# Optimization experiments

Hardware: AMD Instinct MI355X
Metric: run time of the kernel (lower is better)

The kernel has to match this reference:

```python
import jax, jax.numpy as jnp
import numpy as np

B = 4096
IN_DIMS = (3, 32, 32)      # in_numel = 3072
OUT_DIMS = (64, 16, 16)    # out_numel = 16384
IN_NUMEL = int(np.prod(IN_DIMS))
OUT_NUMEL = int(np.prod(OUT_DIMS))


def setup_inputs() -> dict:
    key = jax.random.key(0)
    k1, k2, k3, k4 = jax.random.split(key, 4)
    x = jax.random.normal(k1, (B,) + IN_DIMS, dtype=jnp.float32)
    # Cached composed linear operator (out_numel x in_numel); scale ~1/sqrt(fan_in)
    cached_matrix = jax.random.normal(k2, (OUT_NUMEL, IN_NUMEL), dtype=jnp.float32) / np.sqrt(IN_NUMEL)
    cached_matrix_extra = jax.random.uniform(k3, (1,), dtype=jnp.float32) + 0.5
    cached_tensor_extra = jax.random.normal(k4, (IN_NUMEL, IN_NUMEL), dtype=jnp.float32) / IN_NUMEL
    return {
        "x": x,
        "cached_matrix": cached_matrix,
        "cached_matrix_extra": cached_matrix_extra,
        "cached_tensor_extra": cached_tensor_extra,
    }


def reference(x, cached_matrix, cached_matrix_extra, cached_tensor_extra):
    batches = x.shape[0]
    # input_as_matrix: [in_numel, B]
    X = x.reshape(batches, -1).T
    # input_as_matrix_extra: L2 norm per column -> [1, B]
    X_extra = jnp.linalg.norm(X, ord=2, axis=0, keepdims=True)
    # output_as_matrix = M @ X : [out_numel, B]
    Y = jnp.matmul(cached_matrix, X)
    # output_as_matrix_extra = s * ||x|| + sum((T @ X) * X, axis=0)
    Y_extra = cached_matrix_extra * X_extra + jnp.sum(jnp.matmul(cached_tensor_extra, X) * X, axis=0, keepdims=True)
    Y = Y / Y_extra
    return Y.T.reshape(batches, *OUT_DIMS)
```

## Files before the change

kernel.cpp:

```cpp
#include <hip/hip_runtime.h>
#include <hip/hip_bf16.h>

typedef __attribute__((ext_vector_type(8))) short bf16x8;
typedef __attribute__((ext_vector_type(4))) short bf16x4;
typedef __attribute__((ext_vector_type(4))) float f32x4;

#define DEV __device__ __forceinline__

static constexpr int BATCH = 4096;
static constexpr int KDIM  = 3072;
static constexpr int NOUT  = 16384;

DEV unsigned short f2bf(float f) {
  union { float f; unsigned int u; } v; v.f = f;
  unsigned int u = v.u;
  u += 0x7fffu + ((u >> 16) & 1u);
  return (unsigned short)(u >> 16);
}

DEV float bf2f(unsigned short h) {
  union { unsigned int u; float f; } v;
  v.u = ((unsigned int)h) << 16;
  return v.f;
}

DEV bf16x4 pk4(float4 v) {
  bf16x4 o;
  o[0] = (short)f2bf(v.x); o[1] = (short)f2bf(v.y);
  o[2] = (short)f2bf(v.z); o[3] = (short)f2bf(v.w);
  return o;
}

__global__ __launch_bounds__(256) void prep_cvtT_kernel(
    const float* __restrict__ x, unsigned short* __restrict__ xbf,
    float* __restrict__ nrm,
    const float* __restrict__ T, unsigned short* __restrict__ tbf) {
  __shared__ float red[4];
  const int bid = blockIdx.x;
  const int t = threadIdx.x;
  if (bid < BATCH) {
    const float* row = x + (size_t)bid * KDIM;
    unsigned short* orow = xbf + (size_t)bid * KDIM;
    float ss = 0.f;
#pragma unroll
    for (int i = 0; i < 3; ++i) {
      const int c = i * 256 + t;
      float4 v = reinterpret_cast<const float4*>(row)[c];
      ss += v.x * v.x + v.y * v.y + v.z * v.z + v.w * v.w;
      reinterpret_cast<bf16x4*>(orow)[c] = pk4(v);
    }
#pragma unroll
    for (int off = 32; off > 0; off >>= 1) ss += __shfl_down(ss, off, 64);
    if ((t & 63) == 0) red[t >> 6] = ss;
    __syncthreads();
    if (t == 0) nrm[bid] = sqrtf(red[0] + red[1] + red[2] + red[3]);
  } else {
    const int cb = bid - BATCH;
    const size_t n4 = (size_t)KDIM * KDIM / 4;
    const size_t stride = 1024 * 256;
    for (size_t i = (size_t)cb * 256 + t; i < n4; i += stride) {
      float4 v = reinterpret_cast<const float4*>(T)[i];
      reinterpret_cast<bf16x4*>(tbf)[i] = pk4(v);
    }
  }
}

__global__ __launch_bounds__(256) void finalize_ye_kernel(
    const float* __restrict__ nrm, const float* __restrict__ partial,
    const float* __restrict__ sp, float* __restrict__ ye) {
  const int b = blockIdx.x * blockDim.x + threadIdx.x;
  if (b >= BATCH) return;
  float qv = 0.f;
#pragma unroll
  for (int i = 0; i < 48; ++i) qv += partial[(size_t)b * 48 + i];
  ye[b] = sp[0] * nrm[b] + qv;
}

static constexpr int BK8 = 64;

#define LDSE(BUF, OP, HALF) ((BUF)*32768 + (OP)*16384 + (HALF)*8192)

#define STAGE8(OP, HALF, S, BUF)                                             \
  {                                                                          \
    const unsigned short* gb_ = (OP) ? Bm : A;                               \
    const int gr0_ = ((OP) ? col0 : row0) + (HALF)*128;                      \
    _Pragma("unroll")                                                        \
    for (int j_ = 0; j_ < 2; ++j_) {                                         \
      const int row_ = j_*64 + wid*8 + (lane >> 3);                          \
      const int le_  = ((lane & 7)*8) ^ ((row_ & 7) << 3);                   \
      __builtin_amdgcn_global_load_lds(                                      \
        (const __attribute__((address_space(1))) unsigned int*)(const void*) \
          (gb_ + (size_t)(gr0_ + row_)*KDIM + (S)*BK8 + le_),                \
        (__attribute__((address_space(3))) unsigned int*)(void*)             \
          (lds + LDSE(BUF, OP, HALF) + j_*4096 + wid*512),                   \
        16, 0, 0);                                                           \
    }                                                                        \
  }

#define LOADA8(P, QM, DST)                                                   \
  _Pragma("unroll")                                                          \
  for (int mi = 0; mi < 4; ++mi) {                                           \
    const int r_ = wm*64 + mi*16 + (lane & 15);                              \
    const int xv_ = (r_ & 7) << 3;                                           \
    _Pragma("unroll")                                                        \
    for (int ks = 0; ks < 2; ++ks)                                           \
      DST[mi][ks] = *reinterpret_cast<const bf16x8*>(                        \
          lds + LDSE(P, 0, QM) + ((r_*64 + ks*32 + (lane >> 4)*8) ^ xv_));   \
  }

#define LOADB8(P, QN, DST)                                                   \
  _Pragma("unroll")                                                          \
  for (int ni = 0; ni < 2; ++ni) {                                           \
    const int r_ = wn*32 + ni*16 + (lane & 15);                              \
    const int xv_ = (r_ & 7) << 3;                                           \
    _Pragma("unroll")                                                        \
    for (int ks = 0; ks < 2; ++ks)                                           \
      DST[ni][ks] = *reinterpret_cast<const bf16x8*>(                        \
          lds + LDSE(P, 1, QN) + ((r_*64 + ks*32 + (lane >> 4)*8) ^ xv_));   \
  }

#define MMA8(QM, QN, ASRC, BSRC)                                             \
  __builtin_amdgcn_s_setprio(1);                                             \
  _Pragma("unroll")                                                          \
  for (int mi = 0; mi < 4; ++mi)                                             \
    _Pragma("unroll")                                                        \
    for (int ni = 0; ni < 2; ++ni)                                           \
      _Pragma("unroll")                                                      \
      for (int ks = 0; ks < 2; ++ks)                                         \
        acc[(QM)*4 + mi][(QN)*2 + ni] =                                      \
            __builtin_amdgcn_mfma_f32_16x16x32_bf16(                         \
                ASRC[mi][ks], BSRC[ni][ks], acc[(QM)*4 + mi][(QN)*2 + ni],   \
                0, 0, 0);                                                    \
  __builtin_amdgcn_s_setprio(0);

#define VMW(N)                                                               \
  asm volatile("s_waitcnt vmcnt(" #N ")" ::: "memory");                      \
  __builtin_amdgcn_sched_barrier(0)

#define BARR __builtin_amdgcn_s_barrier()

#define TILE9(P, T)                                                          \
  LOADA8(P, 0, aft); LOADB8(P, 0, bft0);                                     \
  STAGE8(1, 1, (T)+1, (P)^1);                                                \
  BARR;                                                                      \
  STAGE8(1, 0, (T)+1, (P)^1);                                                \
  MMA8(0, 0, aft, bft0);                                                     \
  LOADB8(P, 1, bft1);                                                        \
  BARR;                                                                      \
  STAGE8(0, 0, (T)+2, P);                                                    \
  MMA8(0, 1, aft, bft1);                                                     \
  LOADA8(P, 1, aft);                                                         \
  BARR;                                                                      \
  MMA8(1, 1, aft, bft1);                                                     \
  BARR;                                                                      \
  STAGE8(0, 1, (T)+2, P);                                                    \
  MMA8(1, 0, aft, bft0);                                                     \
  VMW(4);                                                                    \
  BARR;

#define LGKMW8 asm volatile("s_waitcnt lgkmcnt(8)" ::: "memory")

#define TILE8Q(P, T)                                                         \
  LOADA8(P, 0, aft); LOADB8(P, 0, bft0);                                     \
  STAGE8(1, 1, (T)+1, (P)^1);                                                \
  LGKMW8;                                                                    \
  BARR; MMA8(0, 0, aft, bft0); BARR;                                         \
  LOADB8(P, 1, bft1);                                                        \
  STAGE8(1, 0, (T)+1, (P)^1);                                                \
  BARR; MMA8(0, 1, aft, bft1); BARR;                                         \
  LOADA8(P, 1, aft);                                                         \
  STAGE8(0, 0, (T)+2, P);                                                    \
  BARR; MMA8(1, 1, aft, bft1); BARR;                                         \
  STAGE8(0, 1, (T)+2, P);                                                    \
  BARR; MMA8(1, 0, aft, bft0); VMW(4); BARR;

#define PROLOG8Q(T0)                                                         \
  STAGE8(0, 0, (T0), 0); STAGE8(1, 0, (T0), 0);                              \
  STAGE8(0, 1, (T0), 0); STAGE8(1, 1, (T0), 0);                              \
  STAGE8(0, 0, (T0)+1, 1); STAGE8(0, 1, (T0)+1, 1);                          \
  VMW(4);                                                                    \
  BARR;

#define TAIL8Q(TE)                                                           \
  LOADA8(0, 0, aft); LOADB8(0, 0, bft0);                                     \
  STAGE8(1, 1, (TE)+1, 1);                                                   \
  BARR; MMA8(0, 0, aft, bft0); BARR;                                         \
  LOADB8(0, 1, bft1);                                                        \
  STAGE8(1, 0, (TE)+1, 1);                                                   \
  BARR; MMA8(0, 1, aft, bft1); BARR;                                         \
  LOADA8(0, 1, aft);                                                         \
  BARR; MMA8(1, 1, aft, bft1); BARR;                                         \
  MMA8(1, 0, aft, bft0); VMW(0); BARR;                                       \
  LOADA8(1, 0, aft); LOADB8(1, 0, bft0);                                     \
  BARR; MMA8(0, 0, aft, bft0); BARR;                                         \
  LOADB8(1, 1, bft1);                                                        \
  BARR; MMA8(0, 1, aft, bft1); BARR;                                         \
  LOADA8(1, 1, aft);                                                         \
  BARR; MMA8(1, 1, aft, bft1); BARR;                                         \
  MMA8(1, 0, aft, bft0);

__global__ __launch_bounds__(512) void gemm8_kernel(
    const unsigned short* __restrict__ A,
    const unsigned short* __restrict__ Bm,
    const float* __restrict__ ye,
    float* __restrict__ out) {
  __shared__ unsigned short lds[65536];
  const int t = threadIdx.x;
  const int lane = t & 63, wid = t >> 6;
  const int wm = wid >> 2, wn = wid & 3;

  const int bid = blockIdx.x;
  const int xcd = bid & 7, r = bid >> 3;
  const int by = r >> 3;
  const int bx = xcd * 8 + (r & 7);
  const int row0 = by * 256, col0 = bx * 256;

  f32x4 acc[8][4];
#pragma unroll
  for (int i = 0; i < 8; ++i)
#pragma unroll
    for (int j = 0; j < 4; ++j) acc[i][j] = (f32x4){0.f, 0.f, 0.f, 0.f};

  bf16x8 aft[4][2], bft0[2][2], bft1[2][2];

  STAGE8(1, 1, 0, 0); STAGE8(1, 0, 0, 0);
  STAGE8(0, 0, 0, 0); STAGE8(0, 1, 0, 0);
  STAGE8(0, 0, 1, 1); STAGE8(0, 1, 1, 1);
  VMW(4);
  BARR;

#pragma unroll 1
  for (int i = 0; i < 23; ++i) {
    const int t0 = 2 * i;
    TILE9(0, t0);
    TILE9(1, t0 + 1);
  }

  LOADA8(0, 0, aft); LOADB8(0, 0, bft0);
  STAGE8(1, 1, 47, 1);
  BARR;
  STAGE8(1, 0, 47, 1);
  MMA8(0, 0, aft, bft0);
  LOADB8(0, 1, bft1);
  BARR;
  MMA8(0, 1, aft, bft1);
  LOADA8(0, 1, aft);
  BARR;
  MMA8(1, 1, aft, bft1);
  BARR;
  MMA8(1, 0, aft, bft0);
  VMW(0);
  BARR;
  LOADA8(1, 0, aft); LOADB8(1, 0, bft0);
  BARR;
  MMA8(0, 0, aft, bft0);
  LOADB8(1, 1, bft1);
  BARR;
  MMA8(0, 1, aft, bft1);
  LOADA8(1, 1, aft);
  BARR;
  MMA8(1, 1, aft, bft1);
  BARR;
  MMA8(1, 0, aft, bft0);

#pragma unroll
  for (int am = 0; am < 8; ++am) {
#pragma unroll
    for (int j = 0; j < 4; ++j) {
      const int b = row0 + (am >> 2) * 128 + wm * 64 + (am & 3) * 16 +
                    (lane >> 4) * 4 + j;
      const float rr = 1.0f / ye[b];
      float* orow = out + (size_t)b * NOUT + col0;
#pragma unroll
      for (int an = 0; an < 4; ++an)
        orow[(an >> 1) * 128 + wn * 32 + (an & 1) * 16 + (lane & 15)] =
            acc[am][an][j] * rr;
    }
  }
}

#define CVT_EVEN(PT)                                                         \
  if (DOCVT) {                                                               \
    cb0 = Mf4[cvb + (size_t)(((PT)+1)*3    )*512];                           \
    cb1 = Mf4[cvb + (size_t)(((PT)+1)*3 + 1)*512];                           \
    cb2 = Mf4[cvb + (size_t)(((PT)+1)*3 + 2)*512];                           \
    Mb4[cvb + (size_t)((PT)*3    )*512] = pk4(ca0);                          \
    Mb4[cvb + (size_t)((PT)*3 + 1)*512] = pk4(ca1);                          \
    Mb4[cvb + (size_t)((PT)*3 + 2)*512] = pk4(ca2);                          \
  }
#define CVT_ODD(PT)                                                          \
  if (DOCVT) {                                                               \
    ca0 = Mf4[cvb + (size_t)(((PT)+1)*3    )*512];                           \
    ca1 = Mf4[cvb + (size_t)(((PT)+1)*3 + 1)*512];                           \
    if ((PT) != 9) ca2 = Mf4[cvb + (size_t)(((PT)+1)*3 + 2)*512];            \
    Mb4[cvb + (size_t)((PT)*3    )*512] = pk4(cb0);                          \
    Mb4[cvb + (size_t)((PT)*3 + 1)*512] = pk4(cb1);                          \
    Mb4[cvb + (size_t)((PT)*3 + 2)*512] = pk4(cb2);                          \
  }

template <int DOCVT>
__global__ __launch_bounds__(512) void qform8_kernel(
    const unsigned short* __restrict__ A,
    const unsigned short* __restrict__ Bm,
    float* __restrict__ partial,
    const float* __restrict__ Mf,
    unsigned short* __restrict__ Mbf) {
  __shared__ unsigned short lds[65536];
  const int t = threadIdx.x;
  const int lane = t & 63, wid = t >> 6;
  const int wm = wid >> 2, wn = wid & 3;

  const int bid = blockIdx.x;
  const int wgid = (bid & 7) * 96 + (bid >> 3);
  const int jt = wgid / 64;
  const int rem = wgid % 64;
  const int bt = rem >> 2;
  const int ks4 = rem & 3;
  const int row0 = bt * 256, col0 = jt * 256;
  const int k0t = ks4 * 12;

  f32x4 acc[8][4];
#pragma unroll
  for (int i = 0; i < 8; ++i)
#pragma unroll
    for (int j = 0; j < 4; ++j) acc[i][j] = (f32x4){0.f, 0.f, 0.f, 0.f};

  bf16x8 aft[4][2], bft0[2][2], bft1[2][2];

  const float4* Mf4 = reinterpret_cast<const float4*>(Mf);
  bf16x4* Mb4 = reinterpret_cast<bf16x4*>(Mbf);
  const size_t cvb = (size_t)bid * 16384 + t;
  float4 ca0, ca1, ca2, cb0, cb1, cb2;
  if (DOCVT) {
    ca0 = Mf4[cvb];
    ca1 = Mf4[cvb + 512];
    ca2 = Mf4[cvb + 1024];
  }

  PROLOG8Q(k0t);
#pragma unroll 1
  for (int i = 0; i < 5; ++i) {
    const int t0 = k0t + 2 * i;
    CVT_EVEN(2 * i);
    TILE8Q(0, t0);
    CVT_ODD(2 * i + 1);
    TILE8Q(1, t0 + 1);
  }
  if (DOCVT) {
    Mb4[cvb + (size_t)(30) * 512] = pk4(ca0);
    Mb4[cvb + (size_t)(31) * 512] = pk4(ca1);
  }
  TAIL8Q(k0t + 10);

  float* sred = reinterpret_cast<float*>(lds);
#pragma unroll
  for (int am = 0; am < 8; ++am) {
#pragma unroll
    for (int j = 0; j < 4; ++j) {
      const int b = row0 + (am >> 2) * 128 + wm * 64 + (am & 3) * 16 +
                    (lane >> 4) * 4 + j;
      float s = 0.f;
#pragma unroll
      for (int an = 0; an < 4; ++an) {
        const int col = col0 + (an >> 1) * 128 + wn * 32 + (an & 1) * 16 +
                        (lane & 15);
        s += acc[am][an][j] * bf2f(A[(size_t)b * KDIM + col]);
      }
      s += __shfl_xor(s, 1, 64);
      s += __shfl_xor(s, 2, 64);
      s += __shfl_xor(s, 4, 64);
      s += __shfl_xor(s, 8, 64);
      if ((lane & 15) == 0)
        sred[wid * 128 + am * 16 + j * 4 + (lane >> 4)] = s;
    }
  }
  __syncthreads();
  if (t < 256) {
    const int wmI = t >> 7, idx = t & 127;
    const int am = idx >> 4, j = (idx >> 2) & 3, lp = idx & 3;
    const int b = row0 + (am >> 2) * 128 + wmI * 64 + (am & 3) * 16 + lp * 4 + j;
    float s = 0.f;
#pragma unroll
    for (int w2 = 0; w2 < 4; ++w2) s += sred[(wmI * 4 + w2) * 128 + idx];
    partial[(size_t)b * 48 + jt * 4 + ks4] = s;
  }
}

__global__ __launch_bounds__(256) void main_gemm_kernel(
    const unsigned short* __restrict__ A,
    const float* __restrict__ Bf,
    const float* __restrict__ ye,
    float* __restrict__ out) {
  __shared__ unsigned short ldsA[128 * 32];
  __shared__ unsigned short ldsB[128 * 32];
  const int t = threadIdx.x;
  const int lane = t & 63;
  const int wv = t >> 6;
  const int wr = wv >> 1, wc = wv & 1;
  const int col0 = blockIdx.x * 128;
  const int row0 = blockIdx.y * 128;

  f32x4 acc[4][4];
#pragma unroll
  for (int i = 0; i < 4; ++i)
#pragma unroll
    for (int j = 0; j < 4; ++j) acc[i][j] = (f32x4){0.f, 0.f, 0.f, 0.f};

  const unsigned short* aBase = A + (size_t)row0 * KDIM;
  const float* bfBase = Bf + (size_t)col0 * KDIM;
  const int ldsoff0 = (t & ~63) * 8;

  for (int k0 = 0; k0 < KDIM; k0 += 32) {
    __syncthreads();
#pragma unroll
    for (int i = 0; i < 2; ++i) {
      const int c = i * 256 + t;
      const unsigned short* ga = aBase + (size_t)(c >> 2) * KDIM + (k0 + (c & 3) * 8);
      __builtin_amdgcn_global_load_lds(
          (const __attribute__((address_space(1))) unsigned int*)(const void*)ga,
          (__attribute__((address_space(3))) unsigned int*)(void*)(ldsA + i * 2048 + ldsoff0),
          16, 0, 0);
    }
#pragma unroll
    for (int i = 0; i < 2; ++i) {
      const int c = i * 256 + t;
      const int r = c >> 1, ko = (c & 1) * 16;
      const float* gp = bfBase + (size_t)r * KDIM + k0 + ko;
      unsigned short tmp[16];
#pragma unroll
      for (int q = 0; q < 4; ++q) {
        float4 v = reinterpret_cast<const float4*>(gp)[q];
        tmp[q * 4 + 0] = f2bf(v.x); tmp[q * 4 + 1] = f2bf(v.y);
        tmp[q * 4 + 2] = f2bf(v.z); tmp[q * 4 + 3] = f2bf(v.w);
      }
#pragma unroll
      for (int q = 0; q < 2; ++q)
        *reinterpret_cast<bf16x8*>(&ldsB[r * 32 + ko + q * 8]) =
            *reinterpret_cast<const bf16x8*>(&tmp[q * 8]);
    }
    __syncthreads();
    bf16x8 af[4], bfr[4];
#pragma unroll
    for (int mi = 0; mi < 4; ++mi)
      af[mi] = *reinterpret_cast<const bf16x8*>(
          &ldsA[(wr * 64 + mi * 16 + (lane & 15)) * 32 + (lane >> 4) * 8]);
#pragma unroll
    for (int ni = 0; ni < 4; ++ni)
      bfr[ni] = *reinterpret_cast<const bf16x8*>(
          &ldsB[(wc * 64 + ni * 16 + (lane & 15)) * 32 + (lane >> 4) * 8]);
#pragma unroll
    for (int mi = 0; mi < 4; ++mi)
#pragma unroll
      for (int ni = 0; ni < 4; ++ni)
        acc[mi][ni] = __builtin_amdgcn_mfma_f32_16x16x32_bf16(af[mi], bfr[ni], acc[mi][ni], 0, 0, 0);
  }

#pragma unroll
  for (int mi = 0; mi < 4; ++mi) {
#pragma unroll
    for (int j = 0; j < 4; ++j) {
      const int b = row0 + wr * 64 + mi * 16 + (lane >> 4) * 4 + j;
      const float rr = 1.0f / ye[b];
      float* orow = out + (size_t)b * NOUT + col0 + wc * 64 + (lane & 15);
#pragma unroll
      for (int ni = 0; ni < 4; ++ni) orow[ni * 16] = acc[mi][ni][j] * rr;
    }
  }
}

extern "C" void kernel_launch(void* const* d_in, const int* in_sizes, int n_in,
                              void* d_out, int out_size, void* d_ws, size_t ws_size,
                              hipStream_t stream) {
  (void)in_sizes; (void)n_in; (void)out_size;
  const float* x  = (const float*)d_in[0];
  const float* M  = (const float*)d_in[1];
  const float* sc = (const float*)d_in[2];
  const float* T  = (const float*)d_in[3];
  float* out = (float*)d_out;
  char* ws = (char*)d_ws;

  size_t off = 0;
  auto wsalloc = [&](size_t bytes) -> void* {
    void* p = ws + off;
    off += (bytes + 255) & ~(size_t)255;
    return p;
  };
  unsigned short* Xbf = (unsigned short*)wsalloc((size_t)BATCH * KDIM * 2);
  unsigned short* Tbf = (unsigned short*)wsalloc((size_t)KDIM * KDIM * 2);
  float* nrm = (float*)wsalloc((size_t)BATCH * 4);
  float* ye  = (float*)wsalloc((size_t)BATCH * 4);
  float* partial = (float*)wsalloc((size_t)BATCH * 48 * 4);
  unsigned short* Mbf = (unsigned short*)wsalloc((size_t)NOUT * KDIM * 2);
  const bool useMbf = (off <= ws_size);

  prep_cvtT_kernel<<<BATCH + 1024, 256, 0, stream>>>(x, Xbf, nrm, T, Tbf);
  if (useMbf)
    qform8_kernel<1><<<768, 512, 0, stream>>>(Xbf, Tbf, partial, M, Mbf);
  else
    qform8_kernel<0><<<768, 512, 0, stream>>>(Xbf, Tbf, partial, M, Mbf);
  finalize_ye_kernel<<<BATCH / 256, 256, 0, stream>>>(nrm, partial, sc, ye);
  if (useMbf)
    gemm8_kernel<<<1024, 512, 0, stream>>>(Xbf, Mbf, ye, out);
  else
    main_gemm_kernel<<<dim3(NOUT / 128, BATCH / 128), 256, 0, stream>>>(
        Xbf, M, ye, out);
}
```

Before: 558.2 us.

## Replace 8-wave quadrant-pipelined GEMM with simple double-buffered full-tile loop

Replaces the main bf16 GEMM's intricate quadrant-interleaved schedule, which staged and computed tile halves with many barriers, with a plain double-buffered loop. Each iteration prefetches the next K tile into the other LDS buffer via global_load_lds, waits, then runs the full 8x4 MFMA block per wave in two k-steps. The wave-to-tile mapping changes so each wave owns a contiguous 128x64 output region. The goal is to cut barrier count and scheduling complexity, at the cost of less fine-grained overlap between LDS loads and MFMAs and a full barrier each iteration.

```diff
diff --git a/kernel.cpp b/kernel.cpp
--- a/kernel.cpp
+++ b/kernel.cpp
@@ -139,24 +139,7 @@
 
 #define BARR __builtin_amdgcn_s_barrier()
 
-#define TILE9(P, T)                                                          \
-  LOADA8(P, 0, aft); LOADB8(P, 0, bft0);                                     \
-  STAGE8(1, 1, (T)+1, (P)^1);                                                \
-  BARR;                                                                      \
-  STAGE8(1, 0, (T)+1, (P)^1);                                                \
-  MMA8(0, 0, aft, bft0);                                                     \
-  LOADB8(P, 1, bft1);                                                        \
-  BARR;                                                                      \
-  STAGE8(0, 0, (T)+2, P);                                                    \
-  MMA8(0, 1, aft, bft1);                                                     \
-  LOADA8(P, 1, aft);                                                         \
-  BARR;                                                                      \
-  MMA8(1, 1, aft, bft1);                                                     \
-  BARR;                                                                      \
-  STAGE8(0, 1, (T)+2, P);                                                    \
-  MMA8(1, 0, aft, bft0);                                                     \
-  VMW(4);                                                                    \
-  BARR;
+#define SBAR0 __builtin_amdgcn_sched_barrier(0)
 
 #define LGKMW8 asm volatile("s_waitcnt lgkmcnt(8)" ::: "memory")
 
@@ -199,7 +182,54 @@
   BARR; MMA8(1, 1, aft, bft1); BARR;                                         \
   MMA8(1, 0, aft, bft0);
 
-__global__ __launch_bounds__(512) void gemm8_kernel(
+#define LDS2(BUF, OP) ((BUF)*32768 + (OP)*16384)
+
+#define STAGE2(OP, S, BUF)                                                   \
+  {                                                                          \
+    const unsigned short* gb_ = (OP) ? Bm : A;                               \
+    const int gr0_ = (OP) ? col0 : row0;                                     \
+    _Pragma("unroll")                                                        \
+    for (int j_ = 0; j_ < 4; ++j_) {                                         \
+      const int row_ = j_*64 + wid*8 + (lane >> 3);                          \
+      const int le_  = ((lane & 7)*8) ^ ((row_ & 7) << 3);                   \
+      __builtin_amdgcn_global_load_lds(                                      \
+        (const __attribute__((address_space(1))) unsigned int*)(const void*) \
+          (gb_ + (size_t)(gr0_ + row_)*KDIM + (S)*BK8 + le_),                \
+        (__attribute__((address_space(3))) unsigned int*)(void*)             \
+          (lds + LDS2(BUF, OP) + j_*4096 + wid*512),                         \
+        16, 0, 0);                                                           \
+    }                                                                        \
+  }
+
+#define LOADA2(P, KS)                                                        \
+  _Pragma("unroll")                                                          \
+  for (int mi = 0; mi < 8; ++mi) {                                           \
+    const int r_ = wm*128 + mi*16 + (lane & 15);                             \
+    aft[mi] = *reinterpret_cast<const bf16x8*>(                              \
+        lds + LDS2(P, 0) +                                                   \
+        ((r_*64 + (KS)*32 + (lane >> 4)*8) ^ ((r_ & 7) << 3)));              \
+  }
+
+#define LOADB2(P, KS)                                                        \
+  _Pragma("unroll")                                                          \
+  for (int ni = 0; ni < 4; ++ni) {                                           \
+    const int r_ = wn*64 + ni*16 + (lane & 15);                              \
+    bft[ni] = *reinterpret_cast<const bf16x8*>(                              \
+        lds + LDS2(P, 1) +                                                   \
+        ((r_*64 + (KS)*32 + (lane >> 4)*8) ^ ((r_ & 7) << 3)));              \
+  }
+
+#define MMA2                                                                 \
+  __builtin_amdgcn_s_setprio(1);                                             \
+  _Pragma("unroll")                                                          \
+  for (int mi = 0; mi < 8; ++mi)                                             \
+    _Pragma("unroll")                                                        \
+    for (int ni = 0; ni < 4; ++ni)                                           \
+      acc[mi][ni] = __builtin_amdgcn_mfma_f32_16x16x32_bf16(                 \
+          aft[mi], bft[ni], acc[mi][ni], 0, 0, 0);                           \
+  __builtin_amdgcn_s_setprio(0);
+
+__global__ __launch_bounds__(512) void gemm2b_kernel(
     const unsigned short* __restrict__ A,
     const unsigned short* __restrict__ Bm,
     const float* __restrict__ ye,
@@ -221,60 +251,41 @@
 #pragma unroll
     for (int j = 0; j < 4; ++j) acc[i][j] = (f32x4){0.f, 0.f, 0.f, 0.f};
 
-  bf16x8 aft[4][2], bft0[2][2], bft1[2][2];
-
-  STAGE8(1, 1, 0, 0); STAGE8(1, 0, 0, 0);
-  STAGE8(0, 0, 0, 0); STAGE8(0, 1, 0, 0);
-  STAGE8(0, 0, 1, 1); STAGE8(0, 1, 1, 1);
-  VMW(4);
-  BARR;
+  bf16x8 aft[8], bft[4];
+
+  STAGE2(0, 0, 0); STAGE2(1, 0, 0);
 
 #pragma unroll 1
-  for (int i = 0; i < 23; ++i) {
-    const int t0 = 2 * i;
-    TILE9(0, t0);
-    TILE9(1, t0 + 1);
-  }
-
-  LOADA8(0, 0, aft); LOADB8(0, 0, bft0);
-  STAGE8(1, 1, 47, 1);
-  BARR;
-  STAGE8(1, 0, 47, 1);
-  MMA8(0, 0, aft, bft0);
-  LOADB8(0, 1, bft1);
-  BARR;
-  MMA8(0, 1, aft, bft1);
-  LOADA8(0, 1, aft);
-  BARR;
-  MMA8(1, 1, aft, bft1);
-  BARR;
-  MMA8(1, 0, aft, bft0);
+  for (int kt = 0; kt < 47; ++kt) {
+    const int bn = (kt + 1) & 1;
+    STAGE2(0, kt + 1, bn); STAGE2(1, kt + 1, bn);
+    VMW(8);
+    BARR;
+    const int p = kt & 1;
+    LOADA2(p, 0); LOADB2(p, 0);
+    MMA2;
+    SBAR0;
+    LOADA2(p, 1); LOADB2(p, 1);
+    MMA2;
+    BARR;
+  }
   VMW(0);
   BARR;
-  LOADA8(1, 0, aft); LOADB8(1, 0, bft0);
-  BARR;
-  MMA8(0, 0, aft, bft0);
-  LOADB8(1, 1, bft1);
-  BARR;
-  MMA8(0, 1, aft, bft1);
-  LOADA8(1, 1, aft);
-  BARR;
-  MMA8(1, 1, aft, bft1);
-  BARR;
-  MMA8(1, 0, aft, bft0);
-
-#pragma unroll
-  for (int am = 0; am < 8; ++am) {
+  LOADA2(1, 0); LOADB2(1, 0);
+  MMA2;
+  SBAR0;
+  LOADA2(1, 1); LOADB2(1, 1);
+  MMA2;
+
+#pragma unroll
+  for (int mi = 0; mi < 8; ++mi) {
 #pragma unroll
     for (int j = 0; j < 4; ++j) {
-      const int b = row0 + (am >> 2) * 128 + wm * 64 + (am & 3) * 16 +
-                    (lane >> 4) * 4 + j;
+      const int b = row0 + wm * 128 + mi * 16 + (lane >> 4) * 4 + j;
       const float rr = 1.0f / ye[b];
-      float* orow = out + (size_t)b * NOUT + col0;
-#pragma unroll
-      for (int an = 0; an < 4; ++an)
-        orow[(an >> 1) * 128 + wn * 32 + (an & 1) * 16 + (lane & 15)] =
-            acc[am][an][j] * rr;
+      float* orow = out + (size_t)b * NOUT + col0 + wn * 64 + (lane & 15);
+#pragma unroll
+      for (int ni = 0; ni < 4; ++ni) orow[ni * 16] = acc[mi][ni][j] * rr;
     }
   }
 }
@@ -500,7 +511,7 @@
     qform8_kernel<0><<<768, 512, 0, stream>>>(Xbf, Tbf, partial, M, Mbf);
   finalize_ye_kernel<<<BATCH / 256, 256, 0, stream>>>(nrm, partial, sc, ye);
   if (useMbf)
-    gemm8_kernel<<<1024, 512, 0, stream>>>(Xbf, Mbf, ye, out);
+    gemm2b_kernel<<<1024, 512, 0, stream>>>(Xbf, Mbf, ye, out);
   else
     main_gemm_kernel<<<dim3(NOUT / 128, BATCH / 128), 256, 0, stream>>>(
         Xbf, M, ye, out);
```

After: 600.1 us. +7.5%, slower.
